# Performance work log

Measured on AMD Instinct MI355X. Metric: run time of the kernel, lower is better.

## Reference

```python
import jax, jax.numpy as jnp
import numpy as np

T, B, H, K = 512, 64, 512, 16  # seq_len, batch, hidden_size, num_tags


def setup_inputs() -> dict:
    key = jax.random.key(0)
    ks = jax.random.split(key, 8)
    hidden = jax.random.normal(ks[0], (T, B, H), dtype=jnp.float32)
    W1 = jax.random.normal(ks[1], (H, H), dtype=jnp.float32) / np.float32(np.sqrt(H))
    b1 = jnp.zeros((H,), jnp.float32)
    W2 = jax.random.normal(ks[2], (H, K), dtype=jnp.float32) / np.float32(np.sqrt(H))
    b2 = jnp.zeros((K,), jnp.float32)
    transition = jax.random.normal(ks[3], (K, K), dtype=jnp.float32)
    lens = jax.random.randint(ks[4], (B,), T // 2, T + 1)  # valid lengths in [T/2, T]
    tags = jax.random.randint(ks[5], (T, B), 0, K)
    return dict(hidden=hidden, W1=W1, b1=b1, W2=W2, b2=b2,
                transition=transition, lens=lens, tags=tags)


def reference(hidden, W1, b1, W2, b2, transition, lens, tags):
    # Emission MLP (dropout is identity in eval): Linear -> ReLU -> Linear
    h = jax.nn.relu(hidden @ W1 + b1)          # [T, B, H]
    em = h @ W2 + b2                           # [T, B, K]

    # ---- forward (partition) score: linear-chain logsumexp DP ----
    def step(alpha, e_t):
        # alpha: [B, K] over prev tags; transition[curr, prev]
        a = jax.nn.logsumexp(alpha[:, None, :] + transition[None, :, :], axis=-1) + e_t
        return a, a

    alpha0 = em[0]
    _, alphas = jax.lax.scan(step, alpha0, em[1:])
    alphas = jnp.concatenate([alpha0[None], alphas], axis=0)            # [T, B, K]
    last = jnp.take_along_axis(alphas, (lens - 1)[None, :, None], axis=0)[0]  # [B, K]
    fwd_score = jax.nn.logsumexp(last, axis=-1)                          # [B]

    # ---- gold path score ----
    em_path = jnp.take_along_axis(em, tags[:, :, None], axis=-1)[..., 0]  # [T, B]
    trans_path = transition[tags[1:], tags[:-1]]                          # [T-1, B]
    steps = em_path.at[1:].add(trans_path)
    cum = jnp.cumsum(steps, axis=0)                                       # [T, B]
    gold = jnp.take_along_axis(cum, (lens - 1)[None, :], axis=0)[0]       # [B]

    return (fwd_score - gold).sum()
```

## Files before the change

### kernel.cpp

```cpp
#include <hip/hip_runtime.h>
#include <hip/hip_bf16.h>

#define TT 512
#define BB 64
#define HH 512
#define KK 16

typedef __attribute__((ext_vector_type(8))) short bf16x8;
typedef __attribute__((ext_vector_type(4))) short bf16x4;
typedef __attribute__((ext_vector_type(4))) float f32x4;

#define MFMA_K16(A, B, C) __builtin_amdgcn_mfma_f32_16x16x16bf16_1k(A, B, C, 0, 0, 0)

__device__ __forceinline__ unsigned short f2bf(float f) {
    union { __hip_bfloat16 h; unsigned short u; } cvt;
    cvt.h = __float2bfloat16(f);
    return cvt.u;
}

__device__ __forceinline__ short rne_bf(float x) {
    unsigned u = __float_as_uint(x);
    u += 0x7fffu + ((u >> 16) & 1u);
    return (short)(u >> 16);
}

__device__ __forceinline__ float bf2f(short s) {
    return __uint_as_float(((unsigned)(unsigned short)s) << 16);
}

__global__ void prep_kernel(const float* __restrict__ W1, const float* __restrict__ W2,
                            unsigned short* __restrict__ W1t, unsigned short* __restrict__ W2t,
                            float* __restrict__ out) {
    const int bi = blockIdx.x, tx = threadIdx.x;
    if (bi < 64) {
        __shared__ float Ls[64][65];
        const int ti = bi & 7, tj = bi >> 3;
        const int r0 = ti * 64, c0 = tj * 64;
        const int r = tx >> 4, c4 = (tx & 15) * 4;
#pragma unroll
        for (int i = 0; i < 4; ++i) {
            float4 v = *(const float4*)(W1 + (size_t)(r0 + r + 16 * i) * HH + c0 + c4);
            Ls[c4 + 0][r + 16 * i] = v.x;
            Ls[c4 + 1][r + 16 * i] = v.y;
            Ls[c4 + 2][r + 16 * i] = v.z;
            Ls[c4 + 3][r + 16 * i] = v.w;
        }
        __syncthreads();
        const int rn = tx >> 4, k4 = (tx & 15) * 4;
#pragma unroll
        for (int i = 0; i < 4; ++i) {
            const int n = rn + 16 * i;
            ushort4 o;
            o.x = f2bf(Ls[n][k4 + 0]);
            o.y = f2bf(Ls[n][k4 + 1]);
            o.z = f2bf(Ls[n][k4 + 2]);
            o.w = f2bf(Ls[n][k4 + 3]);
            *(ushort4*)(W1t + (size_t)(c0 + n) * HH + r0 + k4) = o;
        }
    } else {
        if (tx == 0) out[0] = 0.0f;
        for (int idx = tx; idx < 16 * HH; idx += 256) {
            const int n = idx >> 9, k = idx & 511;
            W2t[idx] = f2bf(W2[k * KK + n]);
        }
    }
}

__global__ __launch_bounds__(256, 2)
void em_kernel(const float* __restrict__ hidden, const unsigned short* __restrict__ W1t,
               const float* __restrict__ b1, const unsigned short* __restrict__ W2t,
               const float* __restrict__ b2, float* __restrict__ em) {
    __shared__ unsigned short W2ts[16 * 520];
    __shared__ __align__(16) unsigned char stage[37888];
    unsigned short* As = (unsigned short*)stage;
    unsigned short* Bs = (unsigned short*)(stage + 5120);
    unsigned short* Hb = (unsigned short*)stage;

    const int tx = threadIdx.x;
    const int w = tx >> 6, lane = tx & 63;
    const int q = lane >> 4, nl = lane & 15;
    const int wm = w >> 1, wn = w & 1;
    const int row0 = blockIdx.x * 64;

    for (int i = tx; i < 16 * 64; i += 256) {
        const int n = i >> 6, kc = i & 63;
        *(bf16x8*)(W2ts + n * 520 + kc * 8) = *(const bf16x8*)(W2t + n * HH + kc * 8);
    }

    f32x4 acc[2][16];
#pragma unroll
    for (int mt = 0; mt < 2; ++mt)
#pragma unroll
        for (int nt = 0; nt < 16; ++nt) acc[mt][nt] = (f32x4){0.f, 0.f, 0.f, 0.f};

    for (int kt = 0; kt < 16; ++kt) {
        const int k0 = kt * 32;
        __syncthreads();
        {
            const int r = tx >> 2, c8 = (tx & 3) * 8;
            const float* src = hidden + (size_t)(row0 + r) * HH + k0 + c8;
            float4 v0 = *(const float4*)(src);
            float4 v1 = *(const float4*)(src + 4);
            bf16x8 o;
            o[0] = (short)f2bf(v0.x); o[1] = (short)f2bf(v0.y);
            o[2] = (short)f2bf(v0.z); o[3] = (short)f2bf(v0.w);
            o[4] = (short)f2bf(v1.x); o[5] = (short)f2bf(v1.y);
            o[6] = (short)f2bf(v1.z); o[7] = (short)f2bf(v1.w);
            *(bf16x8*)(As + r * 40 + c8) = o;
        }
#pragma unroll
        for (int it = 0; it < 8; ++it) {
            const int c = it * 256 + tx;
            const int n = c >> 2, slot = c & 3;
            const int kc = slot ^ ((n >> 1) & 3);
            __builtin_amdgcn_global_load_lds(
                (const __attribute__((address_space(1))) void*)(W1t + (size_t)n * HH + k0 + kc * 8),
                (__attribute__((address_space(3))) void*)(Bs + c * 8),
                16, 0, 0);
        }
        __syncthreads();
        bf16x8 af[2];
#pragma unroll
        for (int mt = 0; mt < 2; ++mt)
            af[mt] = *(const bf16x8*)(As + (32 * wm + 16 * mt + nl) * 40 + q * 8);
#pragma unroll
        for (int nt = 0; nt < 16; ++nt) {
            const int n = 256 * wn + 16 * nt + nl;
            const int slot = q ^ ((n >> 1) & 3);
            bf16x8 bf = *(const bf16x8*)(Bs + n * 32 + slot * 8);
            acc[0][nt] = __builtin_amdgcn_mfma_f32_16x16x32_bf16(af[0], bf, acc[0][nt], 0, 0, 0);
            acc[1][nt] = __builtin_amdgcn_mfma_f32_16x16x32_bf16(af[1], bf, acc[1][nt], 0, 0, 0);
        }
    }

    f32x4 acc2 = (f32x4){0.f, 0.f, 0.f, 0.f};
    for (int c = 0; c < 2; ++c) {
        __syncthreads();
        if (wn == c) {
#pragma unroll
            for (int nt = 0; nt < 16; ++nt) {
                const float bv = b1[c * 256 + 16 * nt + nl];
#pragma unroll
                for (int mt = 0; mt < 2; ++mt) {
#pragma unroll
                    for (int r = 0; r < 4; ++r) {
                        float v = acc[mt][nt][r] + bv;
                        v = v > 0.f ? v : 0.f;
                        const int row = 32 * wm + 16 * mt + q * 4 + r;
                        Hb[row * 264 + nt * 16 + nl] = f2bf(v);
                    }
                }
            }
        }
        __syncthreads();
#pragma unroll
        for (int ks = 0; ks < 8; ++ks) {
            bf16x8 a2 = *(const bf16x8*)(Hb + (16 * w + nl) * 264 + ks * 32 + q * 8);
            bf16x8 b2f = *(const bf16x8*)(W2ts + nl * 520 + c * 256 + ks * 32 + q * 8);
            acc2 = __builtin_amdgcn_mfma_f32_16x16x32_bf16(a2, b2f, acc2, 0, 0, 0);
        }
    }
#pragma unroll
    for (int r = 0; r < 4; ++r) {
        const int row = row0 + 16 * w + q * 4 + r;
        em[(size_t)row * KK + nl] = acc2[r] + b2[nl];
    }
}

__global__ void gold_kernel(const float* __restrict__ em, const float* __restrict__ trans,
                            const int* __restrict__ lens, const int* __restrict__ tags,
                            float* __restrict__ out) {
    __shared__ float trs[256];
    __shared__ float red[4];
    const int tid = threadIdx.x;
    trs[tid] = __logf(bf2f(rne_bf(__expf(trans[tid]))));
    __syncthreads();
    const int idx = blockIdx.x * 256 + tid;
    const int t = idx >> 6, b = idx & 63;
    const int L = lens[b];
    float v = 0.0f;
    if (t < L) {
        const int tg = tags[t * BB + b];
        v = em[((size_t)t * BB + b) * KK + tg];
        if (t > 0) v += trs[tg * 16 + tags[(t - 1) * BB + b]];
    }
#pragma unroll
    for (int dd = 1; dd < 64; dd <<= 1) v += __shfl_xor(v, dd, 64);
    if ((tid & 63) == 0) red[tid >> 6] = v;
    __syncthreads();
    if (tid == 0) atomicAdd(out, -(red[0] + red[1] + red[2] + red[3]));
}

__global__ void chunk_kernel(const float* __restrict__ em, const float* __restrict__ trans,
                             const int* __restrict__ lens,
                             float* __restrict__ Pfull, float* __restrict__ Cfull,
                             float* __restrict__ Ppart, float* __restrict__ Cpart) {
    const int tx = threadIdx.x;
    const int id = blockIdx.x * 4 + (tx >> 6);
    const int lane = tx & 63, q = lane >> 4, col = lane & 15;
    const int b = id >> 3, c = id & 7;

    float mf[4];
    {
        float4 tv = *(const float4*)(trans + col * 16 + 4 * q);
        mf[0] = bf2f(rne_bf(__expf(tv.x)));
        mf[1] = bf2f(rne_bf(__expf(tv.y)));
        mf[2] = bf2f(rne_bf(__expf(tv.z)));
        mf[3] = bf2f(rne_bf(__expf(tv.w)));
    }
    const int Lm1 = lens[b] - 1;
    const int tb0 = 64 * c;

    float ebuf[8];
#pragma unroll
    for (int i = 0; i < 8; ++i)
        ebuf[i] = em[(size_t)((tb0 + i) * BB + b) * KK + col];

    bf16x4 gb;
#pragma unroll
    for (int i = 0; i < 4; ++i)
        gb[i] = (4 * q + i == col) ? rne_bf(1.0f) : (short)0;

    const f32x4 zc = (f32x4){0.f, 0.f, 0.f, 0.f};
    f32x4 d = (f32x4){0.f, 0.f, 0.f, 0.f};
    float K = 1.0f, rk = 1.0f, lk = 0.0f, Cacc = 0.0f;

    for (int sb = 0; sb < 64; sb += 8) {
        const bool refill = (sb < 56);
#pragma unroll
        for (int s8 = 0; s8 < 8; ++s8) {
            const int t = tb0 + sb + s8;
            const float eraw = ebuf[s8];
            if (refill)
                ebuf[s8] = em[(size_t)((t + 8) * BB + b) * KK + col];
            float ev = __expf(eraw);
            if ((s8 & 3) == 0 && (sb + s8) >= 4) {
                ev *= rk;
                Cacc += lk;
            }
            bf16x4 af;
            af[0] = rne_bf(ev * mf[0]); af[1] = rne_bf(ev * mf[1]);
            af[2] = rne_bf(ev * mf[2]); af[3] = rne_bf(ev * mf[3]);
            if (s8 == 0) {
                if (sb == 0 && c == 0) {
#pragma unroll
                    for (int i = 0; i < 4; ++i)
                        af[i] = (4 * q + i == col) ? rne_bf(ev) : (short)0;
                }
            }
            d = MFMA_K16(af, gb, zc);
            if ((s8 & 3) == 1) {
                K = __shfl(d[0], 0, 64);
                const float Km = fmaxf(K, 1e-30f);
                rk = 1.0f / Km;
                lk = __logf(Km);
            }
            if (t == Lm1) {
#pragma unroll
                for (int r = 0; r < 4; ++r)
                    Ppart[b * 256 + (4 * q + r) * 16 + col] = d[r];
                if (lane == 0) Cpart[b] = Cacc;
            }
            gb[0] = rne_bf(d[0]); gb[1] = rne_bf(d[1]);
            gb[2] = rne_bf(d[2]); gb[3] = rne_bf(d[3]);
        }
    }
#pragma unroll
    for (int r = 0; r < 4; ++r)
        Pfull[(size_t)(b * 8 + c) * 256 + (4 * q + r) * 16 + col] = d[r];
    if (lane == 0) Cfull[b * 8 + c] = Cacc;
}

__global__ void combine_kernel(const int* __restrict__ lens,
                               const float* __restrict__ Pfull, const float* __restrict__ Cfull,
                               const float* __restrict__ Ppart, const float* __restrict__ Cpart,
                               float* __restrict__ out) {
    const int lane = threadIdx.x;
    const int grp = lane >> 4, j = lane & 15;
    const int b = blockIdx.x * 4 + grp;
    const int base = grp << 4;
    const int cstar = (lens[b] - 1) >> 6;

    float g = 1.0f, acc = 0.0f;
    for (int c = 0; c < 8; ++c) {
        const bool act = (c <= cstar);
        const float* P = (c < cstar) ? (Pfull + (size_t)(b * 8 + c) * 256)
                                     : (Ppart + b * 256);
        float gn = 0.0f;
#pragma unroll
        for (int k = 0; k < 16; ++k) {
            const float gk = __shfl(g, base + k, 64);
            gn += P[j * 16 + k] * gk;
        }
        if (act) {
            float m = gn;
#pragma unroll
            for (int dd = 1; dd < 16; dd <<= 1) m = fmaxf(m, __shfl_xor(m, dd, 64));
            g = gn / m;
            acc += __logf(m) + ((c < cstar) ? Cfull[b * 8 + c] : Cpart[b]);
        }
    }
    float ssum = g;
#pragma unroll
    for (int dd = 1; dd < 16; dd <<= 1) ssum += __shfl_xor(ssum, dd, 64);
    const float fwd = acc + __logf(ssum);
    if (j == 0) atomicAdd(out, fwd);
}

extern "C" void kernel_launch(void* const* d_in, const int* in_sizes, int n_in,
                              void* d_out, int out_size, void* d_ws, size_t ws_size,
                              hipStream_t stream) {
    const float* hidden = (const float*)d_in[0];
    const float* W1     = (const float*)d_in[1];
    const float* b1     = (const float*)d_in[2];
    const float* W2     = (const float*)d_in[3];
    const float* b2     = (const float*)d_in[4];
    const float* trans  = (const float*)d_in[5];
    const int*   lens   = (const int*)d_in[6];
    const int*   tags   = (const int*)d_in[7];
    float* out = (float*)d_out;

    char* ws = (char*)d_ws;
    float* em = (float*)ws;
    unsigned short* W1t = (unsigned short*)(ws + 2097152);
    unsigned short* W2t = (unsigned short*)(ws + 2621440);
    float* Pfull = (float*)(ws + 2637824);
    float* Cfull = (float*)(ws + 3162112);
    float* Ppart = (float*)(ws + 3164160);
    float* Cpart = (float*)(ws + 3229696);

    prep_kernel<<<65, 256, 0, stream>>>(W1, W2, W1t, W2t, out);
    em_kernel<<<512, 256, 0, stream>>>(hidden, W1t, b1, W2t, b2, em);
    gold_kernel<<<128, 256, 0, stream>>>(em, trans, lens, tags, out);
    chunk_kernel<<<128, 256, 0, stream>>>(em, trans, lens, Pfull, Cfull, Ppart, Cpart);
    combine_kernel<<<16, 64, 0, stream>>>(lens, Pfull, Cfull, Ppart, Cpart, out);
}
```

Measured before the change: 165.2 us.

## Double-buffer hidden and W1 tiles in em_kernel to overlap loads with MFMA

Turns the em_kernel K-loop into a double-buffered pipeline. The next hidden tile is loaded into registers and the next W1 tile is sent to LDS via global_load_lds while the current tile's MFMAs run, so each step needs one barrier instead of two. W2 staging moves after the main loop so it can reuse LDS. LDS use grows to about 75KB per block, which may limit the two-blocks-per-CU occupancy the launch bounds ask for.

```diff
diff --git a/kernel.cpp b/kernel.cpp
--- a/kernel.cpp
+++ b/kernel.cpp
@@ -70,11 +70,7 @@
 void em_kernel(const float* __restrict__ hidden, const unsigned short* __restrict__ W1t,
                const float* __restrict__ b1, const unsigned short* __restrict__ W2t,
                const float* __restrict__ b2, float* __restrict__ em) {
-    __shared__ unsigned short W2ts[16 * 520];
-    __shared__ __align__(16) unsigned char stage[37888];
-    unsigned short* As = (unsigned short*)stage;
-    unsigned short* Bs = (unsigned short*)(stage + 5120);
-    unsigned short* Hb = (unsigned short*)stage;
+    __shared__ __align__(16) unsigned char stage[2 * 37888];
 
     const int tx = threadIdx.x;
     const int w = tx >> 6, lane = tx & 63;
@@ -82,10 +78,7 @@
     const int wm = w >> 1, wn = w & 1;
     const int row0 = blockIdx.x * 64;
 
-    for (int i = tx; i < 16 * 64; i += 256) {
-        const int n = i >> 6, kc = i & 63;
-        *(bf16x8*)(W2ts + n * 520 + kc * 8) = *(const bf16x8*)(W2t + n * HH + kc * 8);
-    }
+    const int ar = tx >> 2, ac8 = (tx & 3) * 8;
 
     f32x4 acc[2][16];
 #pragma unroll
@@ -93,32 +86,57 @@
 #pragma unroll
         for (int nt = 0; nt < 16; ++nt) acc[mt][nt] = (f32x4){0.f, 0.f, 0.f, 0.f};
 
-    for (int kt = 0; kt < 16; ++kt) {
-        const int k0 = kt * 32;
-        __syncthreads();
-        {
-            const int r = tx >> 2, c8 = (tx & 3) * 8;
-            const float* src = hidden + (size_t)(row0 + r) * HH + k0 + c8;
-            float4 v0 = *(const float4*)(src);
-            float4 v1 = *(const float4*)(src + 4);
-            bf16x8 o;
-            o[0] = (short)f2bf(v0.x); o[1] = (short)f2bf(v0.y);
-            o[2] = (short)f2bf(v0.z); o[3] = (short)f2bf(v0.w);
-            o[4] = (short)f2bf(v1.x); o[5] = (short)f2bf(v1.y);
-            o[6] = (short)f2bf(v1.z); o[7] = (short)f2bf(v1.w);
-            *(bf16x8*)(As + r * 40 + c8) = o;
-        }
+    {
+        unsigned short* As0 = (unsigned short*)stage;
+        unsigned short* Bs0 = As0 + 2560;
+        const float* src = hidden + (size_t)(row0 + ar) * HH + ac8;
+        float4 v0 = *(const float4*)(src);
+        float4 v1 = *(const float4*)(src + 4);
+        bf16x8 o;
+        o[0] = (short)f2bf(v0.x); o[1] = (short)f2bf(v0.y);
+        o[2] = (short)f2bf(v0.z); o[3] = (short)f2bf(v0.w);
+        o[4] = (short)f2bf(v1.x); o[5] = (short)f2bf(v1.y);
+        o[6] = (short)f2bf(v1.z); o[7] = (short)f2bf(v1.w);
+        *(bf16x8*)(As0 + ar * 40 + ac8) = o;
 #pragma unroll
         for (int it = 0; it < 8; ++it) {
             const int c = it * 256 + tx;
             const int n = c >> 2, slot = c & 3;
             const int kc = slot ^ ((n >> 1) & 3);
             __builtin_amdgcn_global_load_lds(
-                (const __attribute__((address_space(1))) void*)(W1t + (size_t)n * HH + k0 + kc * 8),
-                (__attribute__((address_space(3))) void*)(Bs + c * 8),
+                (const __attribute__((address_space(1))) void*)(W1t + (size_t)n * HH + kc * 8),
+                (__attribute__((address_space(3))) void*)(Bs0 + c * 8),
                 16, 0, 0);
         }
-        __syncthreads();
+    }
+    __syncthreads();
+
+    for (int kt = 0; kt < 16; ++kt) {
+        unsigned short* As = (unsigned short*)(stage + (kt & 1) * 37888);
+        unsigned short* Bs = As + 2560;
+        unsigned short* An = (unsigned short*)(stage + ((kt + 1) & 1) * 37888);
+        unsigned short* Bn = An + 2560;
+        const bool pf = (kt < 15);
+
+        float4 v0, v1;
+        if (pf) {
+            const float* src = hidden + (size_t)(row0 + ar) * HH + (kt + 1) * 32 + ac8;
+            v0 = *(const float4*)(src);
+            v1 = *(const float4*)(src + 4);
+        }
+        if (pf) {
+            const int k0n = (kt + 1) * 32;
+#pragma unroll
+            for (int it = 0; it < 8; ++it) {
+                const int c = it * 256 + tx;
+                const int n = c >> 2, slot = c & 3;
+                const int kc = slot ^ ((n >> 1) & 3);
+                __builtin_amdgcn_global_load_lds(
+                    (const __attribute__((address_space(1))) void*)(W1t + (size_t)n * HH + k0n + kc * 8),
+                    (__attribute__((address_space(3))) void*)(Bn + c * 8),
+                    16, 0, 0);
+            }
+        }
         bf16x8 af[2];
 #pragma unroll
         for (int mt = 0; mt < 2; ++mt)
@@ -131,6 +149,22 @@
             acc[0][nt] = __builtin_amdgcn_mfma_f32_16x16x32_bf16(af[0], bf, acc[0][nt], 0, 0, 0);
             acc[1][nt] = __builtin_amdgcn_mfma_f32_16x16x32_bf16(af[1], bf, acc[1][nt], 0, 0, 0);
         }
+        if (pf) {
+            bf16x8 o;
+            o[0] = (short)f2bf(v0.x); o[1] = (short)f2bf(v0.y);
+            o[2] = (short)f2bf(v0.z); o[3] = (short)f2bf(v0.w);
+            o[4] = (short)f2bf(v1.x); o[5] = (short)f2bf(v1.y);
+            o[6] = (short)f2bf(v1.z); o[7] = (short)f2bf(v1.w);
+            *(bf16x8*)(An + ar * 40 + ac8) = o;
+        }
+        __syncthreads();
+    }
+
+    unsigned short* W2s = (unsigned short*)(stage + 37888);
+    unsigned short* Hb  = (unsigned short*)stage;
+    for (int i = tx; i < 16 * 64; i += 256) {
+        const int n = i >> 6, kc = i & 63;
+        *(bf16x8*)(W2s + n * 520 + kc * 8) = *(const bf16x8*)(W2t + n * HH + kc * 8);
     }
 
     f32x4 acc2 = (f32x4){0.f, 0.f, 0.f, 0.f};
@@ -156,7 +190,7 @@
 #pragma unroll
         for (int ks = 0; ks < 8; ++ks) {
             bf16x8 a2 = *(const bf16x8*)(Hb + (16 * w + nl) * 264 + ks * 32 + q * 8);
-            bf16x8 b2f = *(const bf16x8*)(W2ts + nl * 520 + c * 256 + ks * 32 + q * 8);
+            bf16x8 b2f = *(const bf16x8*)(W2s + nl * 520 + c * 256 + ks * 32 + q * 8);
             acc2 = __builtin_amdgcn_mfma_f32_16x16x32_bf16(a2, b2f, acc2, 0, 0, 0);
         }
     }
```

After: 161.9 us. -2.0%, faster.

## Double-buffer em_kernel GEMM with 128-row tiles and 512-thread blocks

Applied to the files above, without the earlier changes.

Rewrites the emission GEMM main loop to double-buffer the A (hidden) and B (W1t) tiles in LDS. The next tile's global loads are issued before computing the current one, with explicit waitcnt and barriers in place of per-iteration syncthreads. Tiles grow to 128 rows with 8 waves per block (256 blocks), and each wave covers 64x128 of the output, which improves B reuse. Costs are about 86KB of LDS per block, which limits occupancy, and more accumulator registers per thread.

```diff
diff --git a/kernel.cpp b/kernel.cpp
--- a/kernel.cpp
+++ b/kernel.cpp
@@ -66,105 +66,151 @@
     }
 }
 
-__global__ __launch_bounds__(256, 2)
+__global__ __launch_bounds__(512, 2)
 void em_kernel(const float* __restrict__ hidden, const unsigned short* __restrict__ W1t,
                const float* __restrict__ b1, const unsigned short* __restrict__ W2t,
                const float* __restrict__ b2, float* __restrict__ em) {
-    __shared__ unsigned short W2ts[16 * 520];
-    __shared__ __align__(16) unsigned char stage[37888];
-    unsigned short* As = (unsigned short*)stage;
-    unsigned short* Bs = (unsigned short*)(stage + 5120);
-    unsigned short* Hb = (unsigned short*)stage;
+    __shared__ __align__(16) unsigned char stage[86016];
+    unsigned short* const As0 = (unsigned short*)(stage);
+    unsigned short* const Bs0 = (unsigned short*)(stage + 10240);
+    unsigned short* const As1 = (unsigned short*)(stage + 43008);
+    unsigned short* const Bs1 = (unsigned short*)(stage + 53248);
 
     const int tx = threadIdx.x;
     const int w = tx >> 6, lane = tx & 63;
     const int q = lane >> 4, nl = lane & 15;
-    const int wm = w >> 1, wn = w & 1;
-    const int row0 = blockIdx.x * 64;
-
-    for (int i = tx; i < 16 * 64; i += 256) {
+    const int wm = w >> 2, wn = w & 3;
+    const int row0 = blockIdx.x * 128;
+    const int ar = tx >> 2, ac8 = (tx & 3) * 8;
+
+    f32x4 acc[4][8];
+#pragma unroll
+    for (int mt = 0; mt < 4; ++mt)
+#pragma unroll
+        for (int nt = 0; nt < 8; ++nt) acc[mt][nt] = (f32x4){0.f, 0.f, 0.f, 0.f};
+
+    float4 a0v0, a0v1, a1v0, a1v1;
+
+#define ISSUE_B(KT, BDST)                                                                 \
+    {                                                                                     \
+        const int k0b = (KT) * 32;                                                        \
+        _Pragma("unroll")                                                                 \
+        for (int it = 0; it < 4; ++it) {                                                  \
+            const int c = it * 512 + tx;                                                  \
+            const int n = c >> 2, slot = c & 3;                                           \
+            const int kc = slot ^ ((n >> 1) & 3);                                         \
+            __builtin_amdgcn_global_load_lds(                                             \
+                (const __attribute__((address_space(1))) void*)(W1t + (size_t)n * HH + k0b + kc * 8), \
+                (__attribute__((address_space(3))) void*)((BDST) + c * 8), 16, 0, 0);     \
+        }                                                                                 \
+    }
+
+#define ISSUE_A(KT, V0, V1)                                                               \
+    {                                                                                     \
+        const float* srcA = hidden + (size_t)(row0 + ar) * HH + (KT) * 32 + ac8;          \
+        V0 = *(const float4*)(srcA);                                                      \
+        V1 = *(const float4*)(srcA + 4);                                                  \
+    }
+
+#define WRITE_A(ADST, V0, V1)                                                             \
+    {                                                                                     \
+        bf16x8 o;                                                                         \
+        o[0] = (short)f2bf((V0).x); o[1] = (short)f2bf((V0).y);                           \
+        o[2] = (short)f2bf((V0).z); o[3] = (short)f2bf((V0).w);                           \
+        o[4] = (short)f2bf((V1).x); o[5] = (short)f2bf((V1).y);                           \
+        o[6] = (short)f2bf((V1).z); o[7] = (short)f2bf((V1).w);                           \
+        *(bf16x8*)((ADST) + ar * 40 + ac8) = o;                                           \
+    }
+
+#define COMPUTE(ABUF, BBUF)                                                               \
+    {                                                                                     \
+        bf16x8 af[4];                                                                     \
+        _Pragma("unroll")                                                                 \
+        for (int mt = 0; mt < 4; ++mt)                                                    \
+            af[mt] = *(const bf16x8*)((ABUF) + (64 * wm + 16 * mt + nl) * 40 + q * 8);    \
+        _Pragma("unroll")                                                                 \
+        for (int nt = 0; nt < 8; ++nt) {                                                  \
+            const int n = 128 * wn + 16 * nt + nl;                                        \
+            const int slot = q ^ ((n >> 1) & 3);                                          \
+            bf16x8 bf = *(const bf16x8*)((BBUF) + n * 32 + slot * 8);                     \
+            _Pragma("unroll")                                                             \
+            for (int mt = 0; mt < 4; ++mt)                                                \
+                acc[mt][nt] = __builtin_amdgcn_mfma_f32_16x16x32_bf16(af[mt], bf, acc[mt][nt], 0, 0, 0); \
+        }                                                                                 \
+    }
+
+    ISSUE_B(0, Bs0);
+    ISSUE_A(0, a0v0, a0v1);
+    ISSUE_A(1, a1v0, a1v1);
+    WRITE_A(As0, a0v0, a0v1);
+    asm volatile("s_waitcnt vmcnt(2) lgkmcnt(0)" ::: "memory");
+    __builtin_amdgcn_s_barrier();
+
+    for (int kt = 0; kt < 14; kt += 2) {
+        ISSUE_B(kt + 1, Bs1);
+        ISSUE_A(kt + 2, a0v0, a0v1);
+        COMPUTE(As0, Bs0);
+        WRITE_A(As1, a1v0, a1v1);
+        asm volatile("s_waitcnt vmcnt(2) lgkmcnt(0)" ::: "memory");
+        __builtin_amdgcn_s_barrier();
+        ISSUE_B(kt + 2, Bs0);
+        ISSUE_A(kt + 3, a1v0, a1v1);
+        COMPUTE(As1, Bs1);
+        WRITE_A(As0, a0v0, a0v1);
+        asm volatile("s_waitcnt vmcnt(2) lgkmcnt(0)" ::: "memory");
+        __builtin_amdgcn_s_barrier();
+    }
+    ISSUE_B(15, Bs1);
+    COMPUTE(As0, Bs0);
+    WRITE_A(As1, a1v0, a1v1);
+    asm volatile("s_waitcnt vmcnt(0) lgkmcnt(0)" ::: "memory");
+    __builtin_amdgcn_s_barrier();
+    COMPUTE(As1, Bs1);
+    asm volatile("s_waitcnt lgkmcnt(0)" ::: "memory");
+    __builtin_amdgcn_s_barrier();
+
+    unsigned short* const Hq  = (unsigned short*)stage;
+    unsigned short* const W2s = (unsigned short*)(stage + 36864);
+    for (int i = tx; i < 1024; i += 512) {
         const int n = i >> 6, kc = i & 63;
-        *(bf16x8*)(W2ts + n * 520 + kc * 8) = *(const bf16x8*)(W2t + n * HH + kc * 8);
-    }
-
-    f32x4 acc[2][16];
-#pragma unroll
-    for (int mt = 0; mt < 2; ++mt)
-#pragma unroll
-        for (int nt = 0; nt < 16; ++nt) acc[mt][nt] = (f32x4){0.f, 0.f, 0.f, 0.f};
-
-    for (int kt = 0; kt < 16; ++kt) {
-        const int k0 = kt * 32;
-        __syncthreads();
-        {
-            const int r = tx >> 2, c8 = (tx & 3) * 8;
-            const float* src = hidden + (size_t)(row0 + r) * HH + k0 + c8;
-            float4 v0 = *(const float4*)(src);
-            float4 v1 = *(const float4*)(src + 4);
-            bf16x8 o;
-            o[0] = (short)f2bf(v0.x); o[1] = (short)f2bf(v0.y);
-            o[2] = (short)f2bf(v0.z); o[3] = (short)f2bf(v0.w);
-            o[4] = (short)f2bf(v1.x); o[5] = (short)f2bf(v1.y);
-            o[6] = (short)f2bf(v1.z); o[7] = (short)f2bf(v1.w);
-            *(bf16x8*)(As + r * 40 + c8) = o;
-        }
-#pragma unroll
-        for (int it = 0; it < 8; ++it) {
-            const int c = it * 256 + tx;
-            const int n = c >> 2, slot = c & 3;
-            const int kc = slot ^ ((n >> 1) & 3);
-            __builtin_amdgcn_global_load_lds(
-                (const __attribute__((address_space(1))) void*)(W1t + (size_t)n * HH + k0 + kc * 8),
-                (__attribute__((address_space(3))) void*)(Bs + c * 8),
-                16, 0, 0);
-        }
-        __syncthreads();
-        bf16x8 af[2];
-#pragma unroll
-        for (int mt = 0; mt < 2; ++mt)
-            af[mt] = *(const bf16x8*)(As + (32 * wm + 16 * mt + nl) * 40 + q * 8);
-#pragma unroll
-        for (int nt = 0; nt < 16; ++nt) {
-            const int n = 256 * wn + 16 * nt + nl;
-            const int slot = q ^ ((n >> 1) & 3);
-            bf16x8 bf = *(const bf16x8*)(Bs + n * 32 + slot * 8);
-            acc[0][nt] = __builtin_amdgcn_mfma_f32_16x16x32_bf16(af[0], bf, acc[0][nt], 0, 0, 0);
-            acc[1][nt] = __builtin_amdgcn_mfma_f32_16x16x32_bf16(af[1], bf, acc[1][nt], 0, 0, 0);
-        }
+        *(bf16x8*)(W2s + n * 520 + kc * 8) = *(const bf16x8*)(W2t + n * HH + kc * 8);
     }
 
     f32x4 acc2 = (f32x4){0.f, 0.f, 0.f, 0.f};
-    for (int c = 0; c < 2; ++c) {
-        __syncthreads();
+    for (int c = 0; c < 4; ++c) {
         if (wn == c) {
 #pragma unroll
-            for (int nt = 0; nt < 16; ++nt) {
-                const float bv = b1[c * 256 + 16 * nt + nl];
-#pragma unroll
-                for (int mt = 0; mt < 2; ++mt) {
+            for (int nt = 0; nt < 8; ++nt) {
+                const float bv = b1[c * 128 + 16 * nt + nl];
+#pragma unroll
+                for (int mt = 0; mt < 4; ++mt) {
 #pragma unroll
                     for (int r = 0; r < 4; ++r) {
                         float v = acc[mt][nt][r] + bv;
                         v = v > 0.f ? v : 0.f;
-                        const int row = 32 * wm + 16 * mt + q * 4 + r;
-                        Hb[row * 264 + nt * 16 + nl] = f2bf(v);
+                        Hq[(64 * wm + 16 * mt + q * 4 + r) * 136 + nt * 16 + nl] = f2bf(v);
                     }
                 }
             }
         }
         __syncthreads();
 #pragma unroll
-        for (int ks = 0; ks < 8; ++ks) {
-            bf16x8 a2 = *(const bf16x8*)(Hb + (16 * w + nl) * 264 + ks * 32 + q * 8);
-            bf16x8 b2f = *(const bf16x8*)(W2ts + nl * 520 + c * 256 + ks * 32 + q * 8);
+        for (int ks = 0; ks < 4; ++ks) {
+            bf16x8 a2 = *(const bf16x8*)(Hq + (16 * w + nl) * 136 + ks * 32 + q * 8);
+            bf16x8 b2f = *(const bf16x8*)(W2s + nl * 520 + c * 128 + ks * 32 + q * 8);
             acc2 = __builtin_amdgcn_mfma_f32_16x16x32_bf16(a2, b2f, acc2, 0, 0, 0);
         }
+        __syncthreads();
     }
 #pragma unroll
     for (int r = 0; r < 4; ++r) {
         const int row = row0 + 16 * w + q * 4 + r;
         em[(size_t)row * KK + nl] = acc2[r] + b2[nl];
     }
+#undef ISSUE_B
+#undef ISSUE_A
+#undef WRITE_A
+#undef COMPUTE
 }
 
 __global__ void gold_kernel(const float* __restrict__ em, const float* __restrict__ trans,
@@ -330,7 +376,7 @@
     float* Cpart = (float*)(ws + 3229696);
 
     prep_kernel<<<65, 256, 0, stream>>>(W1, W2, W1t, W2t, out);
-    em_kernel<<<512, 256, 0, stream>>>(hidden, W1t, b1, W2t, b2, em);
+    em_kernel<<<256, 512, 0, stream>>>(hidden, W1t, b1, W2t, b2, em);
     gold_kernel<<<128, 256, 0, stream>>>(em, trans, lens, tags, out);
     chunk_kernel<<<128, 256, 0, stream>>>(em, trans, lens, Pfull, Cfull, Ppart, Cpart);
     combine_kernel<<<16, 64, 0, stream>>>(lens, Pfull, Cfull, Ppart, Cpart, out);
```

After: 165.3 us. No clear change (+0.1%).

## Halve em tile rows, raise occupancy, and split CRF scan into more chunks

Applied to the files above, without the earlier changes.

The emission GEMM now uses 32-row tiles with each of four waves covering a 128-column slice, which doubles the grid to 1024 blocks and raises launch bounds to 4 blocks per CU. W2 is staged into shared memory after the main loop so its buffer reuses the staging space. The CRF forward scan is split into 32 chunks of 16 steps instead of 8 chunks of 64, which gives four times more chunk blocks and shortens each serial chain. In exchange, each W1 tile is reloaded by twice as many blocks, only two waves do the second GEMM, and the combine kernel has a longer serial matrix-vector chain.

```diff
diff --git a/kernel.cpp b/kernel.cpp
--- a/kernel.cpp
+++ b/kernel.cpp
@@ -5,6 +5,9 @@
 #define BB 64
 #define HH 512
 #define KK 16
+
+#define NCH 32
+#define CST (TT / NCH)
 
 typedef __attribute__((ext_vector_type(8))) short bf16x8;
 typedef __attribute__((ext_vector_type(4))) short bf16x4;
@@ -66,48 +69,29 @@
     }
 }
 
-__global__ __launch_bounds__(256, 2)
+__global__ __launch_bounds__(256, 4)
 void em_kernel(const float* __restrict__ hidden, const unsigned short* __restrict__ W1t,
                const float* __restrict__ b1, const unsigned short* __restrict__ W2t,
                const float* __restrict__ b2, float* __restrict__ em) {
-    __shared__ unsigned short W2ts[16 * 520];
-    __shared__ __align__(16) unsigned char stage[37888];
-    unsigned short* As = (unsigned short*)stage;
-    unsigned short* Bs = (unsigned short*)(stage + 5120);
-    unsigned short* Hb = (unsigned short*)stage;
+    __shared__ __align__(16) unsigned char stage[35328];
+    unsigned short* const As = (unsigned short*)stage;
+    unsigned short* const Bs = (unsigned short*)(stage + 2560);
 
     const int tx = threadIdx.x;
     const int w = tx >> 6, lane = tx & 63;
     const int q = lane >> 4, nl = lane & 15;
-    const int wm = w >> 1, wn = w & 1;
-    const int row0 = blockIdx.x * 64;
-
-    for (int i = tx; i < 16 * 64; i += 256) {
-        const int n = i >> 6, kc = i & 63;
-        *(bf16x8*)(W2ts + n * 520 + kc * 8) = *(const bf16x8*)(W2t + n * HH + kc * 8);
-    }
-
-    f32x4 acc[2][16];
+    const int row0 = blockIdx.x * 32;
+    const int ar = tx >> 3, ac4 = (tx & 7) * 4;
+
+    f32x4 acc[2][8];
 #pragma unroll
     for (int mt = 0; mt < 2; ++mt)
 #pragma unroll
-        for (int nt = 0; nt < 16; ++nt) acc[mt][nt] = (f32x4){0.f, 0.f, 0.f, 0.f};
+        for (int nt = 0; nt < 8; ++nt) acc[mt][nt] = (f32x4){0.f, 0.f, 0.f, 0.f};
 
     for (int kt = 0; kt < 16; ++kt) {
         const int k0 = kt * 32;
         __syncthreads();
-        {
-            const int r = tx >> 2, c8 = (tx & 3) * 8;
-            const float* src = hidden + (size_t)(row0 + r) * HH + k0 + c8;
-            float4 v0 = *(const float4*)(src);
-            float4 v1 = *(const float4*)(src + 4);
-            bf16x8 o;
-            o[0] = (short)f2bf(v0.x); o[1] = (short)f2bf(v0.y);
-            o[2] = (short)f2bf(v0.z); o[3] = (short)f2bf(v0.w);
-            o[4] = (short)f2bf(v1.x); o[5] = (short)f2bf(v1.y);
-            o[6] = (short)f2bf(v1.z); o[7] = (short)f2bf(v1.w);
-            *(bf16x8*)(As + r * 40 + c8) = o;
-        }
 #pragma unroll
         for (int it = 0; it < 8; ++it) {
             const int c = it * 256 + tx;
@@ -115,17 +99,23 @@
             const int kc = slot ^ ((n >> 1) & 3);
             __builtin_amdgcn_global_load_lds(
                 (const __attribute__((address_space(1))) void*)(W1t + (size_t)n * HH + k0 + kc * 8),
-                (__attribute__((address_space(3))) void*)(Bs + c * 8),
-                16, 0, 0);
+                (__attribute__((address_space(3))) void*)(Bs + c * 8), 16, 0, 0);
+        }
+        {
+            float4 v = *(const float4*)(hidden + (size_t)(row0 + ar) * HH + k0 + ac4);
+            ushort4 o;
+            o.x = f2bf(v.x); o.y = f2bf(v.y);
+            o.z = f2bf(v.z); o.w = f2bf(v.w);
+            *(ushort4*)(As + ar * 40 + ac4) = o;
         }
         __syncthreads();
         bf16x8 af[2];
 #pragma unroll
         for (int mt = 0; mt < 2; ++mt)
-            af[mt] = *(const bf16x8*)(As + (32 * wm + 16 * mt + nl) * 40 + q * 8);
-#pragma unroll
-        for (int nt = 0; nt < 16; ++nt) {
-            const int n = 256 * wn + 16 * nt + nl;
+            af[mt] = *(const bf16x8*)(As + (16 * mt + nl) * 40 + q * 8);
+#pragma unroll
+        for (int nt = 0; nt < 8; ++nt) {
+            const int n = 128 * w + 16 * nt + nl;
             const int slot = q ^ ((n >> 1) & 3);
             bf16x8 bf = *(const bf16x8*)(Bs + n * 32 + slot * 8);
             acc[0][nt] = __builtin_amdgcn_mfma_f32_16x16x32_bf16(af[0], bf, acc[0][nt], 0, 0, 0);
@@ -133,37 +123,41 @@
         }
     }
 
-    f32x4 acc2 = (f32x4){0.f, 0.f, 0.f, 0.f};
-    for (int c = 0; c < 2; ++c) {
-        __syncthreads();
-        if (wn == c) {
-#pragma unroll
-            for (int nt = 0; nt < 16; ++nt) {
-                const float bv = b1[c * 256 + 16 * nt + nl];
-#pragma unroll
-                for (int mt = 0; mt < 2; ++mt) {
-#pragma unroll
-                    for (int r = 0; r < 4; ++r) {
-                        float v = acc[mt][nt][r] + bv;
-                        v = v > 0.f ? v : 0.f;
-                        const int row = 32 * wm + 16 * mt + q * 4 + r;
-                        Hb[row * 264 + nt * 16 + nl] = f2bf(v);
-                    }
-                }
-            }
-        }
-        __syncthreads();
-#pragma unroll
-        for (int ks = 0; ks < 8; ++ks) {
-            bf16x8 a2 = *(const bf16x8*)(Hb + (16 * w + nl) * 264 + ks * 32 + q * 8);
-            bf16x8 b2f = *(const bf16x8*)(W2ts + nl * 520 + c * 256 + ks * 32 + q * 8);
+    __syncthreads();
+    unsigned short* const W2s = (unsigned short*)stage;
+    unsigned short* const Hb  = (unsigned short*)(stage + 16640);
+#pragma unroll
+    for (int i = tx; i < 1024; i += 256) {
+        const int n = i >> 6, kc = i & 63;
+        *(bf16x8*)(W2s + n * 520 + kc * 8) = *(const bf16x8*)(W2t + n * HH + kc * 8);
+    }
+#pragma unroll
+    for (int nt = 0; nt < 8; ++nt) {
+        const float bv = b1[128 * w + 16 * nt + nl];
+#pragma unroll
+        for (int mt = 0; mt < 2; ++mt) {
+#pragma unroll
+            for (int r = 0; r < 4; ++r) {
+                float v = acc[mt][nt][r] + bv;
+                v = v > 0.f ? v : 0.f;
+                Hb[(16 * mt + q * 4 + r) * 264 + 128 * w + 16 * nt + nl] = f2bf(v);
+            }
+        }
+    }
+    __syncthreads();
+    if (w < 2) {
+        f32x4 acc2 = (f32x4){0.f, 0.f, 0.f, 0.f};
+#pragma unroll
+        for (int ks = 0; ks < 16; ++ks) {
+            bf16x8 a2  = *(const bf16x8*)(Hb + (16 * w + nl) * 264 + ks * 32 + q * 8);
+            bf16x8 b2f = *(const bf16x8*)(W2s + nl * 520 + ks * 32 + q * 8);
             acc2 = __builtin_amdgcn_mfma_f32_16x16x32_bf16(a2, b2f, acc2, 0, 0, 0);
         }
-    }
-#pragma unroll
-    for (int r = 0; r < 4; ++r) {
-        const int row = row0 + 16 * w + q * 4 + r;
-        em[(size_t)row * KK + nl] = acc2[r] + b2[nl];
+#pragma unroll
+        for (int r = 0; r < 4; ++r) {
+            const int row = row0 + 16 * w + q * 4 + r;
+            em[(size_t)row * KK + nl] = acc2[r] + b2[nl];
+        }
     }
 }
 
@@ -198,7 +192,7 @@
     const int tx = threadIdx.x;
     const int id = blockIdx.x * 4 + (tx >> 6);
     const int lane = tx & 63, q = lane >> 4, col = lane & 15;
-    const int b = id >> 3, c = id & 7;
+    const int b = id >> 5, c = id & 31;
 
     float mf[4];
     {
@@ -209,7 +203,7 @@
         mf[3] = bf2f(rne_bf(__expf(tv.w)));
     }
     const int Lm1 = lens[b] - 1;
-    const int tb0 = 64 * c;
+    const int tb0 = CST * c;
 
     float ebuf[8];
 #pragma unroll
@@ -225,8 +219,8 @@
     f32x4 d = (f32x4){0.f, 0.f, 0.f, 0.f};
     float K = 1.0f, rk = 1.0f, lk = 0.0f, Cacc = 0.0f;
 
-    for (int sb = 0; sb < 64; sb += 8) {
-        const bool refill = (sb < 56);
+    for (int sb = 0; sb < CST; sb += 8) {
+        const bool refill = (sb < CST - 8);
 #pragma unroll
         for (int s8 = 0; s8 < 8; ++s8) {
             const int t = tb0 + sb + s8;
@@ -267,8 +261,8 @@
     }
 #pragma unroll
     for (int r = 0; r < 4; ++r)
-        Pfull[(size_t)(b * 8 + c) * 256 + (4 * q + r) * 16 + col] = d[r];
-    if (lane == 0) Cfull[b * 8 + c] = Cacc;
+        Pfull[(size_t)(b * NCH + c) * 256 + (4 * q + r) * 16 + col] = d[r];
+    if (lane == 0) Cfull[b * NCH + c] = Cacc;
 }
 
 __global__ void combine_kernel(const int* __restrict__ lens,
@@ -279,12 +273,12 @@
     const int grp = lane >> 4, j = lane & 15;
     const int b = blockIdx.x * 4 + grp;
     const int base = grp << 4;
-    const int cstar = (lens[b] - 1) >> 6;
+    const int cstar = (lens[b] - 1) / CST;
 
     float g = 1.0f, acc = 0.0f;
-    for (int c = 0; c < 8; ++c) {
+    for (int c = 0; c < NCH; ++c) {
         const bool act = (c <= cstar);
-        const float* P = (c < cstar) ? (Pfull + (size_t)(b * 8 + c) * 256)
+        const float* P = (c < cstar) ? (Pfull + (size_t)(b * NCH + c) * 256)
                                      : (Ppart + b * 256);
         float gn = 0.0f;
 #pragma unroll
@@ -297,7 +291,7 @@
 #pragma unroll
             for (int dd = 1; dd < 16; dd <<= 1) m = fmaxf(m, __shfl_xor(m, dd, 64));
             g = gn / m;
-            acc += __logf(m) + ((c < cstar) ? Cfull[b * 8 + c] : Cpart[b]);
+            acc += __logf(m) + ((c < cstar) ? Cfull[b * NCH + c] : Cpart[b]);
         }
     }
     float ssum = g;
@@ -325,13 +319,13 @@
     unsigned short* W1t = (unsigned short*)(ws + 2097152);
     unsigned short* W2t = (unsigned short*)(ws + 2621440);
     float* Pfull = (float*)(ws + 2637824);
-    float* Cfull = (float*)(ws + 3162112);
-    float* Ppart = (float*)(ws + 3164160);
-    float* Cpart = (float*)(ws + 3229696);
+    float* Cfull = (float*)(ws + 4734976);
+    float* Ppart = (float*)(ws + 4743168);
+    float* Cpart = (float*)(ws + 4808704);
 
     prep_kernel<<<65, 256, 0, stream>>>(W1, W2, W1t, W2t, out);
-    em_kernel<<<512, 256, 0, stream>>>(hidden, W1t, b1, W2t, b2, em);
+    em_kernel<<<1024, 256, 0, stream>>>(hidden, W1t, b1, W2t, b2, em);
     gold_kernel<<<128, 256, 0, stream>>>(em, trans, lens, tags, out);
-    chunk_kernel<<<128, 256, 0, stream>>>(em, trans, lens, Pfull, Cfull, Ppart, Cpart);
+    chunk_kernel<<<512, 256, 0, stream>>>(em, trans, lens, Pfull, Cfull, Ppart, Cpart);
     combine_kernel<<<16, 64, 0, stream>>>(lens, Pfull, Cfull, Ppart, Cpart, out);
 }
```

After: 173.7 us. 5.1% more time.
